# Performance work log

Measured on AMD Instinct MI355X. Metric: run time of the kernel, lower is better.

The kernel has to match this reference:

```python
import jax, jax.numpy as jnp
import numpy as np

B, N, K, C = 4, 4096, 32, 192  # batch, npoint, nsample, channels (C % 6 == 0)
EPS = 1e-5


def setup_inputs() -> dict:
    key = jax.random.key(0)
    ks = jax.random.split(key, 8)
    p = jax.random.normal(ks[0], (B, N, 3), jnp.float32)
    x = jax.random.normal(ks[1], (B, C, N), jnp.float32)
    idx = jax.random.randint(ks[2], (B, N, K), 0, N)  # ball-query neighbor ids
    W = jax.random.normal(ks[3], (C, C + 3), jnp.float32) * 0.05  # 1x1 conv weight
    gamma = 1.0 + 0.1 * jax.random.normal(ks[4], (C,), jnp.float32)
    beta = 0.1 * jax.random.normal(ks[5], (C,), jnp.float32)
    rmean = 0.1 * jax.random.normal(ks[6], (C,), jnp.float32)
    rvar = jax.random.uniform(ks[7], (C,), jnp.float32) + 0.5  # positive running var
    return dict(p=p, x=x, idx=idx, W=W, gamma=gamma, beta=beta, rmean=rmean, rvar=rvar)


def reference(p, x, idx, W, gamma, beta, rmean, rvar):
    # --- grouper: gather neighbors, relative coords ---
    pn = jax.vmap(lambda pp, ii: pp[ii])(p, idx)            # [B,N,K,3]
    dp = jnp.transpose(pn - p[:, :, None, :], (0, 3, 1, 2))  # [B,3,N,K]
    xj = jax.vmap(lambda xx, ii: xx[:, ii])(x, idx)          # [B,C,N,K]
    # --- PosPool sin/cos positional embedding fused with features ---
    feat_dim = C // 6
    dim_mat = jnp.power(500.0, jnp.arange(feat_dim, dtype=jnp.float32) / feat_dim)
    div = (50.0 * dp)[..., None] / dim_mat                   # [B,3,N,K,fd]
    pe = jnp.concatenate([jnp.sin(div), jnp.cos(div)], axis=-1)  # [B,3,N,K,2fd]
    pe = jnp.transpose(pe, (0, 1, 4, 2, 3)).reshape(B, C, N, K)  # [B,C,N,K]
    agg = xj * pe + pe
    # --- dp_fj concat -> 1x1 conv -> BN(eval) -> ReLU ---
    h = jnp.concatenate([dp, agg], axis=1)                   # [B,C+3,N,K]
    y = jnp.einsum('oc,bcnk->bonk', W, h)                    # [B,C,N,K]
    inv = gamma / jnp.sqrt(rvar + EPS)
    y = y * inv[:, None, None] + (beta - rmean * inv)[:, None, None]
    y = jax.nn.relu(y)
    # --- max reduction over neighbors ---
    return jnp.max(y, axis=-1)                               # [B,C,N]
```

## Files before the change

kernel.cpp:

```cpp
#include <hip/hip_runtime.h>
#include <math.h>

#define B_   4
#define N_   4096
#define K_   32
#define C_   192
#define CH_  195
#define KPAD 224
#define PTS  2
#define NKT  7
#define NNT  4
#define GRID ((B_ * N_) / PTS)

using half8  = __attribute__((ext_vector_type(8))) _Float16;
using half2v = __attribute__((ext_vector_type(2))) _Float16;
using f32x4  = __attribute__((ext_vector_type(4))) float;

__device__ _Float16 g_Wp[C_ * KPAD];
__device__ _Float16 g_xT[(size_t)B_ * N_ * C_];

__device__ __forceinline__ float dpp_max16(float v) {
    int s;
    s = __builtin_amdgcn_update_dpp(0, __float_as_int(v), 0xB1,  0xF, 0xF, true);
    v = fmaxf(v, __int_as_float(s));
    s = __builtin_amdgcn_update_dpp(0, __float_as_int(v), 0x4E,  0xF, 0xF, true);
    v = fmaxf(v, __int_as_float(s));
    s = __builtin_amdgcn_update_dpp(0, __float_as_int(v), 0x141, 0xF, 0xF, true);
    v = fmaxf(v, __int_as_float(s));
    s = __builtin_amdgcn_update_dpp(0, __float_as_int(v), 0x140, 0xF, 0xF, true);
    v = fmaxf(v, __int_as_float(s));
    return v;
}

__global__ __launch_bounds__(256) void prep(const float* __restrict__ x,
                                            const float* __restrict__ W,
                                            const float* __restrict__ gamma_,
                                            const float* __restrict__ rvar) {
    __shared__ float s[32][97];
    const int tid = threadIdx.x;
    if (blockIdx.x < 1024) {
        const int bi = blockIdx.x;
        const int b  = bi >> 8;
        const int c0 = ((bi >> 7) & 1) * 96;
        const int n0 = (bi & 127) * 32;
#pragma unroll
        for (int it = 0; it < 3; ++it) {
            const int c  = it * 32 + (tid >> 3);
            const int n4 = (tid & 7) * 4;
            const float4 v = *(const float4*)(x + ((size_t)b * C_ + c0 + c) * N_ + n0 + n4);
            s[n4 + 0][c] = v.x; s[n4 + 1][c] = v.y; s[n4 + 2][c] = v.z; s[n4 + 3][c] = v.w;
        }
        __syncthreads();
#pragma unroll
        for (int it = 0; it < 2; ++it) {
            const int t = it * 256 + tid;
            if (t < 32 * 12) {
                const int n  = t / 12;
                const int ch = t - n * 12;
                half8 v;
#pragma unroll
                for (int jj = 0; jj < 8; ++jj) v[jj] = (_Float16)s[n][ch * 8 + jj];
                *(half8*)(g_xT + ((size_t)b * N_ + n0 + n) * C_ + c0 + ch * 8) = v;
            }
        }
    } else {
        const int i = (blockIdx.x - 1024) * 256 + tid;
        if (i < C_ * KPAD) {
            const int o = i / KPAD, r = i - o * KPAD;
            const float inv = gamma_[o] * rsqrtf(rvar[o] + 1e-5f);
            float v = 0.0f;
            if (r < 3)                  v = W[o * CH_ + r];
            else if (r >= 8 && r < 200) v = W[o * CH_ + 3 + (r - 8)];
            g_Wp[i] = (_Float16)(v * inv);
        }
    }
}

__global__ __launch_bounds__(256, 5) void la_mfma(
    const float* __restrict__ p,
    const int*   __restrict__ idx,
    const float* __restrict__ gamma_,
    const float* __restrict__ beta_,
    const float* __restrict__ rmean,
    const float* __restrict__ rvar,
    float* __restrict__ out)
{
    __shared__ _Float16 hb[NKT * NNT * 64 * 8];
    __shared__ float s_bias[C_], s_fr[32], s_out[C_ * PTS];

    const int tid  = threadIdx.x;
    const int lane = tid & 63;
    const int w    = tid >> 6;
    const int l15  = lane & 15;
    const int quad = lane >> 4;

    const int q  = blockIdx.x & 7;
    const int sI = blockIdx.x >> 3;
    const int L  = q * (GRID / 8) + sI;
    const int bn0 = L * PTS;
    const int b   = bn0 >> 12;
    const int n0  = bn0 & (N_ - 1);

    if (tid < C_) {
        const float inv = gamma_[tid] * rsqrtf(rvar[tid] + 1e-5f);
        s_bias[tid] = beta_[tid] - rmean[tid] * inv;
    }
    if (tid < 32) s_fr[tid] = 7.9577471546f * exp2f(-(float)tid * 0.2801808715263400f);
    __syncthreads();

    {
        const int col = w * 16 + l15;
        const int pt  = col >> 5;
        const int k   = col & 31;
        const int gp  = bn0 + pt;
        const int j   = idx[(size_t)gp * K_ + k];
        const float d0 = p[(size_t)(b * N_ + j) * 3 + 0] - p[(size_t)gp * 3 + 0];
        const float d1 = p[(size_t)(b * N_ + j) * 3 + 1] - p[(size_t)gp * 3 + 1];
        const float d2 = p[(size_t)(b * N_ + j) * 3 + 2] - p[(size_t)gp * 3 + 2];
        const _Float16* xh = g_xT + ((size_t)b * N_ + j) * C_;

        float sfr[8];
#pragma unroll
        for (int jj = 0; jj < 8; ++jj) sfr[jj] = s_fr[quad * 8 + jj];

#pragma unroll
        for (int i6 = 0; i6 < 6; ++i6) {
            const int chunk = quad + 4 * i6;
            const half8 v = *(const half8*)(xh + chunk * 8);
            const float dd  = (chunk < 8) ? d0 : ((chunk < 16) ? d1 : d2);
            const float off = (chunk & 4) ? 0.25f : 0.0f;
            half8 hv;
#pragma unroll
            for (int jj = 0; jj < 8; jj += 2) {
                const float pe0 = __builtin_amdgcn_sinf(fmaf(dd, sfr[jj],     off));
                const float pe1 = __builtin_amdgcn_sinf(fmaf(dd, sfr[jj + 1], off));
                const half2v pe2 = __builtin_bit_cast(half2v, __builtin_amdgcn_cvt_pkrtz(pe0, pe1));
                half2v v2; v2[0] = v[jj]; v2[1] = v[jj + 1];
                const half2v r2 = pe2 * v2 + pe2;
                hv[jj] = r2[0]; hv[jj + 1] = r2[1];
            }
            const int ro = chunk + 1;
            const int kt = ro >> 2, kq = ro & 3;
            *(half8*)(&hb[(size_t)((kt * NNT + w) * 64 + kq * 16 + l15) * 8]) = hv;
        }
        if (quad == 0) {
            half8 hv0 = (half8)(_Float16)0.0f;
            hv0[0] = (_Float16)d0; hv0[1] = (_Float16)d1; hv0[2] = (_Float16)d2;
            *(half8*)(&hb[(size_t)((0 * NNT + w) * 64 + 0 * 16 + l15) * 8]) = hv0;
        } else {
            const int ro = 24 + quad;
            const int kt = ro >> 2, kq = ro & 3;
            *(half8*)(&hb[(size_t)((kt * NNT + w) * 64 + kq * 16 + l15) * 8]) = (half8)(_Float16)0.0f;
        }
    }
    __syncthreads();

    f32x4 acc[3][4];
#pragma unroll
    for (int i = 0; i < 3; ++i)
#pragma unroll
        for (int t = 0; t < 4; ++t) acc[i][t] = (f32x4)0.0f;

#pragma unroll
    for (int kt = 0; kt < NKT; ++kt) {
        const int k0 = kt * 32 + quad * 8;
        half8 a[3], bf[4];
#pragma unroll
        for (int i = 0; i < 3; ++i) {
            const int m = (w * 3 + i) * 16 + l15;
            a[i] = *(const half8*)(g_Wp + (size_t)m * KPAD + k0);
        }
#pragma unroll
        for (int t = 0; t < 4; ++t)
            bf[t] = *(const half8*)(&hb[(size_t)((kt * NNT + t) * 64 + lane) * 8]);
#pragma unroll
        for (int i = 0; i < 3; ++i)
#pragma unroll
            for (int t = 0; t < 4; ++t)
                acc[i][t] = __builtin_amdgcn_mfma_f32_16x16x32_f16(a[i], bf[t], acc[i][t], 0, 0, 0);
    }

#pragma unroll
    for (int i = 0; i < 3; ++i) {
        const int mbase = (w * 3 + i) * 16 + quad * 4;
#pragma unroll
        for (int pt = 0; pt < PTS; ++pt) {
            const f32x4 va = acc[i][2 * pt];
            const f32x4 vb = acc[i][2 * pt + 1];
#pragma unroll
            for (int r = 0; r < 4; ++r) {
                float v = fmaxf(va[r], vb[r]);
                v = dpp_max16(v);
                if (l15 == 0) {
                    const int m = mbase + r;
                    s_out[m * PTS + pt] = fmaxf(v + s_bias[m], 0.0f);
                }
            }
        }
    }
    __syncthreads();

    if (tid < C_) {
        const float2 o2 = *(const float2*)(&s_out[tid * PTS]);
        *(float2*)(&out[((size_t)b * C_ + tid) * N_ + n0]) = o2;
    }
}

extern "C" void kernel_launch(void* const* d_in, const int* in_sizes, int n_in,
                              void* d_out, int out_size, void* d_ws, size_t ws_size,
                              hipStream_t stream) {
    (void)in_sizes; (void)n_in; (void)out_size; (void)d_ws; (void)ws_size;
    const float* p      = (const float*)d_in[0];
    const float* x      = (const float*)d_in[1];
    const int*   idx    = (const int*)d_in[2];
    const float* W      = (const float*)d_in[3];
    const float* gamma_ = (const float*)d_in[4];
    const float* beta_  = (const float*)d_in[5];
    const float* rmean  = (const float*)d_in[6];
    const float* rvar   = (const float*)d_in[7];
    float* out = (float*)d_out;

    prep<<<1024 + (C_ * KPAD + 255) / 256, 256, 0, stream>>>(x, W, gamma_, rvar);
    la_mfma<<<GRID, 256, 0, stream>>>(p, idx, gamma_, beta_, rmean, rvar, out);
}
```

Baseline: 169.9 us.

## Share sin/cos arguments, pack max-reduce in fp16, write outputs directly

The positional-embedding loop now evaluates sin and cos on the same argument instead of using a sin with a quarter-period offset, which halves the argument computations. The neighbor max-reduction packs the two points into one half2 and does a single DPP reduction chain per row. Each row's output is stored straight to global memory, removing the shared-memory staging and the final barrier. The prep transpose also reads shared memory as float4 with a padded row stride. Rounding the max to fp16 before adding the bias loses some precision.

```diff
diff --git a/kernel.cpp b/kernel.cpp
--- a/kernel.cpp
+++ b/kernel.cpp
@@ -19,16 +19,27 @@
 __device__ _Float16 g_Wp[C_ * KPAD];
 __device__ _Float16 g_xT[(size_t)B_ * N_ * C_];
 
-__device__ __forceinline__ float dpp_max16(float v) {
+__device__ __forceinline__ half2v hmax2(half2v a, half2v b) {
+#if __has_builtin(__builtin_elementwise_max)
+    return __builtin_elementwise_max(a, b);
+#else
+    half2v r;
+    r[0] = (a[0] > b[0]) ? a[0] : b[0];
+    r[1] = (a[1] > b[1]) ? a[1] : b[1];
+    return r;
+#endif
+}
+
+__device__ __forceinline__ half2v dpp_hmax16(half2v v) {
     int s;
-    s = __builtin_amdgcn_update_dpp(0, __float_as_int(v), 0xB1,  0xF, 0xF, true);
-    v = fmaxf(v, __int_as_float(s));
-    s = __builtin_amdgcn_update_dpp(0, __float_as_int(v), 0x4E,  0xF, 0xF, true);
-    v = fmaxf(v, __int_as_float(s));
-    s = __builtin_amdgcn_update_dpp(0, __float_as_int(v), 0x141, 0xF, 0xF, true);
-    v = fmaxf(v, __int_as_float(s));
-    s = __builtin_amdgcn_update_dpp(0, __float_as_int(v), 0x140, 0xF, 0xF, true);
-    v = fmaxf(v, __int_as_float(s));
+    s = __builtin_amdgcn_update_dpp(0, __builtin_bit_cast(int, v), 0xB1,  0xF, 0xF, true);
+    v = hmax2(v, __builtin_bit_cast(half2v, s));
+    s = __builtin_amdgcn_update_dpp(0, __builtin_bit_cast(int, v), 0x4E,  0xF, 0xF, true);
+    v = hmax2(v, __builtin_bit_cast(half2v, s));
+    s = __builtin_amdgcn_update_dpp(0, __builtin_bit_cast(int, v), 0x141, 0xF, 0xF, true);
+    v = hmax2(v, __builtin_bit_cast(half2v, s));
+    s = __builtin_amdgcn_update_dpp(0, __builtin_bit_cast(int, v), 0x140, 0xF, 0xF, true);
+    v = hmax2(v, __builtin_bit_cast(half2v, s));
     return v;
 }
 
@@ -36,7 +47,7 @@
                                             const float* __restrict__ W,
                                             const float* __restrict__ gamma_,
                                             const float* __restrict__ rvar) {
-    __shared__ float s[32][97];
+    __shared__ float s[32][100];
     const int tid = threadIdx.x;
     if (blockIdx.x < 1024) {
         const int bi = blockIdx.x;
@@ -57,9 +68,13 @@
             if (t < 32 * 12) {
                 const int n  = t / 12;
                 const int ch = t - n * 12;
+                const float4 f0 = *(const float4*)(&s[n][ch * 8 + 0]);
+                const float4 f1 = *(const float4*)(&s[n][ch * 8 + 4]);
                 half8 v;
-#pragma unroll
-                for (int jj = 0; jj < 8; ++jj) v[jj] = (_Float16)s[n][ch * 8 + jj];
+                v[0] = (_Float16)f0.x; v[1] = (_Float16)f0.y;
+                v[2] = (_Float16)f0.z; v[3] = (_Float16)f0.w;
+                v[4] = (_Float16)f1.x; v[5] = (_Float16)f1.y;
+                v[6] = (_Float16)f1.z; v[7] = (_Float16)f1.w;
                 *(half8*)(g_xT + ((size_t)b * N_ + n0 + n) * C_ + c0 + ch * 8) = v;
             }
         }
@@ -86,7 +101,7 @@
     float* __restrict__ out)
 {
     __shared__ _Float16 hb[NKT * NNT * 64 * 8];
-    __shared__ float s_bias[C_], s_fr[32], s_out[C_ * PTS];
+    __shared__ float s_bias[C_], s_fr[32];
 
     const int tid  = threadIdx.x;
     const int lane = tid & 63;
@@ -124,24 +139,36 @@
         for (int jj = 0; jj < 8; ++jj) sfr[jj] = s_fr[quad * 8 + jj];
 
 #pragma unroll
-        for (int i6 = 0; i6 < 6; ++i6) {
-            const int chunk = quad + 4 * i6;
-            const half8 v = *(const half8*)(xh + chunk * 8);
-            const float dd  = (chunk < 8) ? d0 : ((chunk < 16) ? d1 : d2);
-            const float off = (chunk & 4) ? 0.25f : 0.0f;
-            half8 hv;
+        for (int dp3 = 0; dp3 < 3; ++dp3) {
+            const int cS = quad + 8 * dp3;
+            const int cC = cS + 4;
+            const half8 vS = *(const half8*)(xh + cS * 8);
+            const half8 vC = *(const half8*)(xh + cC * 8);
+            const float dd = (dp3 == 0) ? d0 : ((dp3 == 1) ? d1 : d2);
+            half8 hS, hC;
 #pragma unroll
             for (int jj = 0; jj < 8; jj += 2) {
-                const float pe0 = __builtin_amdgcn_sinf(fmaf(dd, sfr[jj],     off));
-                const float pe1 = __builtin_amdgcn_sinf(fmaf(dd, sfr[jj + 1], off));
-                const half2v pe2 = __builtin_bit_cast(half2v, __builtin_amdgcn_cvt_pkrtz(pe0, pe1));
-                half2v v2; v2[0] = v[jj]; v2[1] = v[jj + 1];
-                const half2v r2 = pe2 * v2 + pe2;
-                hv[jj] = r2[0]; hv[jj + 1] = r2[1];
-            }
-            const int ro = chunk + 1;
-            const int kt = ro >> 2, kq = ro & 3;
-            *(half8*)(&hb[(size_t)((kt * NNT + w) * 64 + kq * 16 + l15) * 8]) = hv;
+                const float a0 = dd * sfr[jj];
+                const float a1 = dd * sfr[jj + 1];
+                const half2v ps = __builtin_bit_cast(half2v, __builtin_amdgcn_cvt_pkrtz(
+                    __builtin_amdgcn_sinf(a0), __builtin_amdgcn_sinf(a1)));
+                const half2v pc = __builtin_bit_cast(half2v, __builtin_amdgcn_cvt_pkrtz(
+                    __builtin_amdgcn_cosf(a0), __builtin_amdgcn_cosf(a1)));
+                half2v vs2; vs2[0] = vS[jj]; vs2[1] = vS[jj + 1];
+                half2v vc2; vc2[0] = vC[jj]; vc2[1] = vC[jj + 1];
+                const half2v rs = ps * vs2 + ps;
+                const half2v rc = pc * vc2 + pc;
+                hS[jj] = rs[0]; hS[jj + 1] = rs[1];
+                hC[jj] = rc[0]; hC[jj + 1] = rc[1];
+            }
+            {
+                const int ro = cS + 1, kt = ro >> 2, kq = ro & 3;
+                *(half8*)(&hb[(size_t)((kt * NNT + w) * 64 + kq * 16 + l15) * 8]) = hS;
+            }
+            {
+                const int ro = cC + 1, kt = ro >> 2, kq = ro & 3;
+                *(half8*)(&hb[(size_t)((kt * NNT + w) * 64 + kq * 16 + l15) * 8]) = hC;
+            }
         }
         if (quad == 0) {
             half8 hv0 = (half8)(_Float16)0.0f;
@@ -184,25 +211,20 @@
     for (int i = 0; i < 3; ++i) {
         const int mbase = (w * 3 + i) * 16 + quad * 4;
 #pragma unroll
-        for (int pt = 0; pt < PTS; ++pt) {
-            const f32x4 va = acc[i][2 * pt];
-            const f32x4 vb = acc[i][2 * pt + 1];
-#pragma unroll
-            for (int r = 0; r < 4; ++r) {
-                float v = fmaxf(va[r], vb[r]);
-                v = dpp_max16(v);
-                if (l15 == 0) {
-                    const int m = mbase + r;
-                    s_out[m * PTS + pt] = fmaxf(v + s_bias[m], 0.0f);
-                }
-            }
-        }
-    }
-    __syncthreads();
-
-    if (tid < C_) {
-        const float2 o2 = *(const float2*)(&s_out[tid * PTS]);
-        *(float2*)(&out[((size_t)b * C_ + tid) * N_ + n0]) = o2;
+        for (int r = 0; r < 4; ++r) {
+            const float y0 = fmaxf(acc[i][0][r], acc[i][1][r]);
+            const float y1 = fmaxf(acc[i][2][r], acc[i][3][r]);
+            half2v h = __builtin_bit_cast(half2v, __builtin_amdgcn_cvt_pkrtz(y0, y1));
+            h = dpp_hmax16(h);
+            if (l15 == 0) {
+                const int m = mbase + r;
+                const float bia = s_bias[m];
+                float2 o2;
+                o2.x = fmaxf((float)h[0] + bia, 0.0f);
+                o2.y = fmaxf((float)h[1] + bia, 0.0f);
+                *(float2*)(out + ((size_t)b * C_ + m) * N_ + n0) = o2;
+            }
+        }
     }
 }
 
```

New measurement: 170.0 us. About the same (+0.0%).
